# Kernel optimization log

Hardware: AMD Instinct MI355X
Metric: run time of the kernel (lower is better)

## Reference

```python
import jax, jax.numpy as jnp
import numpy as np

B, S, D = 2, 2048, 1024
H, DH = 16, 64
FF = 4 * D
EPS = 1e-5
SCALE = 1.0 / np.sqrt(DH)


def setup_inputs() -> dict:
    key = jax.random.key(0)
    ks = jax.random.split(key, 8)
    std = 0.02
    return {
        "x": jax.random.normal(ks[0], (B, S, D), jnp.float32),
        "ln1_g": jnp.ones((D,), jnp.float32),
        "ln1_b": jnp.zeros((D,), jnp.float32),
        "w_qkv": jax.random.normal(ks[1], (D, 3 * H * DH), jnp.float32) * std,
        "b_qkv": jnp.zeros((3 * H * DH,), jnp.float32),
        "w_ao": jax.random.normal(ks[2], (H * DH, D), jnp.float32) * std,
        "b_ao": jnp.zeros((D,), jnp.float32),
        "ln2_g": jnp.ones((D,), jnp.float32),
        "ln2_b": jnp.zeros((D,), jnp.float32),
        "w_fc": jax.random.normal(ks[3], (D, FF), jnp.float32) * std,
        "b_fc": jnp.zeros((FF,), jnp.float32),
        "w_proj": jax.random.normal(ks[4], (FF, D), jnp.float32) * std,
        "b_proj": jnp.zeros((D,), jnp.float32),
    }


def _layernorm(x, g, b):
    mu = jnp.mean(x, axis=-1, keepdims=True)
    var = jnp.mean(jnp.square(x - mu), axis=-1, keepdims=True)
    return (x - mu) * jax.lax.rsqrt(var + EPS) * g + b


def reference(x, ln1_g, ln1_b, w_qkv, b_qkv, w_ao, b_ao,
              ln2_g, ln2_b, w_fc, b_fc, w_proj, b_proj):
    # pre-LN attention
    h = _layernorm(x, ln1_g, ln1_b)
    qkv = h @ w_qkv + b_qkv                      # [B,S,3*H*DH]
    q, k, v = jnp.split(qkv, 3, axis=-1)
    def heads(t):                                 # [B,S,H*DH] -> [B,H,S,DH]
        return t.reshape(B, S, H, DH).transpose(0, 2, 1, 3)
    q, k, v = heads(q), heads(k), heads(v)
    scores = jnp.einsum("bhsd,bhtd->bhst", q, k) * SCALE  # full [B,H,S,S]
    probs = jax.nn.softmax(scores, axis=-1)
    attn = jnp.einsum("bhst,bhtd->bhsd", probs, v)        # [B,H,S,DH]
    attn = attn.transpose(0, 2, 1, 3).reshape(B, S, H * DH)
    attn = attn @ w_ao + b_ao
    x = x + attn
    # pre-LN MLP (exact erf GELU, matches nn.GELU())
    h = _layernorm(x, ln2_g, ln2_b)
    h = jax.nn.gelu(h @ w_fc + b_fc, approximate=False)
    h = h @ w_proj + b_proj
    return x + h
```

## Files before the change

kernel.cpp:

```cpp
#include <hip/hip_runtime.h>
#include <hip/hip_bf16.h>

using short8 = __attribute__((ext_vector_type(8))) short;
using f32x4  = __attribute__((ext_vector_type(4))) float;

#define DEV __device__ __forceinline__

DEV unsigned short f2b(float f) {
  union { float f; unsigned u; } cv; cv.f = f;
  unsigned r = (cv.u + 0x7fffu + ((cv.u >> 16) & 1u)) >> 16;
  return (unsigned short)r;
}

typedef const __attribute__((address_space(1))) unsigned int* gp1;
typedef __attribute__((address_space(3))) unsigned int* lp3;
DEV void gl16(const void* g, void* l) {
  __builtin_amdgcn_global_load_lds((gp1)g, (lp3)l, 16, 0, 0);
}

__global__ void k_tcvt4(const float* __restrict__ s0, unsigned short* __restrict__ d0,
                        const float* __restrict__ s1, unsigned short* __restrict__ d1,
                        const float* __restrict__ s2, unsigned short* __restrict__ d2,
                        const float* __restrict__ s3, unsigned short* __restrict__ d3) {
  __shared__ float tile[32][33];
  int id = blockIdx.x;
  const float* src; unsigned short* dst; int K, N, nx;
  if (id < 3072)      { src = s0; dst = d0; K = 1024; N = 3072; nx = 96; }
  else if (id < 4096) { id -= 3072; src = s1; dst = d1; K = 1024; N = 1024; nx = 32; }
  else if (id < 8192) { id -= 4096; src = s2; dst = d2; K = 1024; N = 4096; nx = 128; }
  else                { id -= 8192; src = s3; dst = d3; K = 4096; N = 1024; nx = 32; }
  int n0 = (id % nx) * 32, k0 = (id / nx) * 32;
  int tx = threadIdx.x, ty = threadIdx.y;
#pragma unroll
  for (int j = 0; j < 4; ++j)
    tile[ty + j * 8][tx] = src[(size_t)(k0 + ty + j * 8) * N + (n0 + tx)];
  __syncthreads();
#pragma unroll
  for (int j = 0; j < 4; ++j)
    dst[(size_t)(n0 + ty + j * 8) * K + (k0 + tx)] = f2b(tile[tx][ty + j * 8]);
}

__global__ void k_tv(const unsigned short* __restrict__ src, unsigned short* __restrict__ dst) {
  __shared__ unsigned short tile[32][33];
  int d0 = blockIdx.x * 32, s0 = blockIdx.y * 32;
  size_t base = (size_t)blockIdx.z * 2048 * 64;
  int tx = threadIdx.x, ty = threadIdx.y;
#pragma unroll
  for (int j = 0; j < 4; ++j)
    tile[ty + j * 8][tx] = src[base + (size_t)(s0 + ty + j * 8) * 64 + (d0 + tx)];
  __syncthreads();
#pragma unroll
  for (int j = 0; j < 4; ++j)
    dst[base + (size_t)(d0 + ty + j * 8) * 2048 + (s0 + tx)] = tile[tx][ty + j * 8];
}

__global__ __launch_bounds__(256) void k_ln(const float* __restrict__ x,
                                            const float* __restrict__ g,
                                            const float* __restrict__ b,
                                            unsigned short* __restrict__ y) {
  int row = blockIdx.x, tid = threadIdx.x;
  float4 v = reinterpret_cast<const float4*>(x + (size_t)row * 1024)[tid];
  float s  = v.x + v.y + v.z + v.w;
  float s2 = v.x * v.x + v.y * v.y + v.z * v.z + v.w * v.w;
#pragma unroll
  for (int m = 1; m < 64; m <<= 1) { s += __shfl_xor(s, m); s2 += __shfl_xor(s2, m); }
  __shared__ float ps[8];
  int w = tid >> 6;
  if ((tid & 63) == 0) { ps[w] = s; ps[4 + w] = s2; }
  __syncthreads();
  s  = ps[0] + ps[1] + ps[2] + ps[3];
  s2 = ps[4] + ps[5] + ps[6] + ps[7];
  float mu   = s * (1.0f / 1024.0f);
  float var  = fmaxf(s2 * (1.0f / 1024.0f) - mu * mu, 0.f);
  float rstd = rsqrtf(var + 1e-5f);
  float4 gv = reinterpret_cast<const float4*>(g)[tid];
  float4 bv = reinterpret_cast<const float4*>(b)[tid];
  ushort4 o;
  o.x = f2b((v.x - mu) * rstd * gv.x + bv.x);
  o.y = f2b((v.y - mu) * rstd * gv.y + bv.y);
  o.z = f2b((v.z - mu) * rstd * gv.z + bv.z);
  o.w = f2b((v.w - mu) * rstd * gv.w + bv.w);
  reinterpret_cast<ushort4*>(y + (size_t)row * 1024)[tid] = o;
}

enum { EPI_QKV = 0, EPI_RESID = 1, EPI_GELU = 2 };

template <int EPI>
__global__ __launch_bounds__(512, 2) void k_gemm256(
    const unsigned short* __restrict__ A, const unsigned short* __restrict__ BT,
    const float* __restrict__ bias, int M, int N, int K,
    unsigned short* __restrict__ outb,
    unsigned short* __restrict__ qb, unsigned short* __restrict__ kb,
    unsigned short* __restrict__ vb) {
  __shared__ __align__(16) unsigned short Abuf[2][256][64];
  __shared__ __align__(16) unsigned short Bbuf[2][256][64];
  int nx = gridDim.x, nwg = nx * gridDim.y;
  int w0 = blockIdx.y * nx + blockIdx.x;
  int id = (w0 & 7) * (nwg >> 3) + (w0 >> 3);
  int bx = id % nx, by = id / nx;
  int m0 = by * 256, n0 = bx * 256;
  int tid = threadIdx.x;
  int lane = tid & 63, wid = tid >> 6;
  int wm = wid >> 2, wn = wid & 3;
  int l15 = lane & 15, g = lane >> 4;
  int swl = l15 & 7;
  int lrow = lane >> 3;
  int lchunk = (lane & 7) ^ lrow;
  const unsigned short* Asrc = A  + (size_t)(m0 + wid * 32 + lrow) * K + lchunk * 8;
  const unsigned short* Bsrc = BT + (size_t)(n0 + wid * 32 + lrow) * K + lchunk * 8;
  auto stage = [&](int buf, int k0) {
#pragma unroll
    for (int i = 0; i < 4; ++i)
      gl16(Asrc + k0 + (size_t)i * 8 * K, &Abuf[buf][wid * 32 + i * 8][0]);
#pragma unroll
    for (int i = 0; i < 4; ++i)
      gl16(Bsrc + k0 + (size_t)i * 8 * K, &Bbuf[buf][wid * 32 + i * 8][0]);
  };
  f32x4 acc[8][4] = {};
  int nt = K >> 6;
  stage(0, 0);
  stage(1, 64);
  asm volatile("s_waitcnt vmcnt(8)" ::: "memory");
  __builtin_amdgcn_sched_barrier(0);
  __builtin_amdgcn_s_barrier();
  int cur = 0;
  for (int t = 0; t < nt; ++t) {
    const unsigned short (*As)[64] = Abuf[cur];
    const unsigned short (*Bs)[64] = Bbuf[cur];
    short8 a0[8], b0[4], a1[8], b1[4];
#pragma unroll
    for (int mi = 0; mi < 8; ++mi)
      a0[mi] = *reinterpret_cast<const short8*>(&As[wm * 128 + mi * 16 + l15][(g ^ swl) * 8]);
#pragma unroll
    for (int ni = 0; ni < 4; ++ni)
      b0[ni] = *reinterpret_cast<const short8*>(&Bs[wn * 64 + ni * 16 + l15][(g ^ swl) * 8]);
    __builtin_amdgcn_s_setprio(1);
#pragma unroll
    for (int mi = 0; mi < 8; ++mi)
#pragma unroll
      for (int ni = 0; ni < 4; ++ni)
        acc[mi][ni] = __builtin_amdgcn_mfma_f32_16x16x32_bf16(a0[mi], b0[ni], acc[mi][ni], 0, 0, 0);
    __builtin_amdgcn_s_setprio(0);
#pragma unroll
    for (int mi = 0; mi < 8; ++mi)
      a1[mi] = *reinterpret_cast<const short8*>(&As[wm * 128 + mi * 16 + l15][((4 + g) ^ swl) * 8]);
#pragma unroll
    for (int ni = 0; ni < 4; ++ni)
      b1[ni] = *reinterpret_cast<const short8*>(&Bs[wn * 64 + ni * 16 + l15][((4 + g) ^ swl) * 8]);
    asm volatile("s_waitcnt lgkmcnt(0)" ::: "memory");
    __builtin_amdgcn_sched_barrier(0);
    __builtin_amdgcn_s_barrier();
    __builtin_amdgcn_sched_barrier(0);
    if (t + 2 < nt) stage(cur, (t + 2) << 6);
    __builtin_amdgcn_s_setprio(1);
#pragma unroll
    for (int mi = 0; mi < 8; ++mi)
#pragma unroll
      for (int ni = 0; ni < 4; ++ni)
        acc[mi][ni] = __builtin_amdgcn_mfma_f32_16x16x32_bf16(a1[mi], b1[ni], acc[mi][ni], 0, 0, 0);
    __builtin_amdgcn_s_setprio(0);
    if (t + 2 < nt) {
      asm volatile("s_waitcnt vmcnt(8)" ::: "memory");
    } else if (t + 1 < nt) {
      asm volatile("s_waitcnt vmcnt(0)" ::: "memory");
    }
    __builtin_amdgcn_sched_barrier(0);
    __builtin_amdgcn_s_barrier();
    cur ^= 1;
  }
#pragma unroll
  for (int mi = 0; mi < 8; ++mi) {
#pragma unroll
    for (int ni = 0; ni < 4; ++ni) {
      int row0 = m0 + wm * 128 + mi * 16 + g * 4;
      int col  = n0 + wn * 64 + ni * 16 + l15;
      float bcol = bias[col];
#pragma unroll
      for (int j = 0; j < 4; ++j) {
        int r = row0 + j;
        float vv = acc[mi][ni][j] + bcol;
        if (EPI == EPI_QKV) {
          int which = col >> 10;
          int hc = col & 1023;
          int h = hc >> 6, d = hc & 63;
          int bb = r >> 11, ss = r & 2047;
          size_t idx = (((size_t)(bb * 16 + h)) * 2048 + ss) * 64 + d;
          unsigned short bv_ = f2b(which == 0 ? vv * 0.18033688011112042f : vv);
          if (which == 0)      qb[idx] = bv_;
          else if (which == 1) kb[idx] = bv_;
          else                 vb[idx] = bv_;
        } else {
          float ge = 0.5f * vv * (1.0f + erff(vv * 0.70710678118654752f));
          outb[(size_t)r * N + col] = f2b(ge);
        }
      }
    }
  }
}

__global__ __launch_bounds__(512) void k_gemm512(
    const unsigned short* __restrict__ A, const unsigned short* __restrict__ BT,
    const float* __restrict__ bias, int M, int N, int K,
    float* __restrict__ outf, const float* __restrict__ resid) {
  __shared__ __align__(16) unsigned short Abuf[2][64][64];
  __shared__ __align__(16) unsigned short Bbuf[2][128][64];
  int nx = gridDim.x, nwg = nx * gridDim.y;
  int w0 = blockIdx.y * nx + blockIdx.x;
  int id = (w0 & 7) * (nwg >> 3) + (w0 >> 3);
  int bx = id % nx, by = id / nx;
  int m0 = by * 64, n0 = bx * 128;
  int tid = threadIdx.x;
  int lane = tid & 63, wid = tid >> 6;
  int wm = wid >> 2, wn = wid & 3;
  int l15 = lane & 15, g = lane >> 4;
  int swl = l15 & 7;
  int lrow = lane >> 3;
  int lchunk = (lane & 7) ^ lrow;
  const unsigned short* Asrc = A  + (size_t)(m0 + wid * 8 + lrow) * K + lchunk * 8;
  const unsigned short* Bsrc = BT + (size_t)(n0 + wid * 16 + lrow) * K + lchunk * 8;
  auto stage = [&](int buf, int k0) {
    gl16(Asrc + k0, &Abuf[buf][wid * 8][0]);
#pragma unroll
    for (int i = 0; i < 2; ++i)
      gl16(Bsrc + k0 + (size_t)i * 8 * K, &Bbuf[buf][wid * 16 + i * 8][0]);
  };
  f32x4 acc[2][2] = {};
  int nt = K >> 6;
  stage(0, 0);
  stage(1, 64);
  asm volatile("s_waitcnt vmcnt(3)" ::: "memory");
  __builtin_amdgcn_sched_barrier(0);
  __builtin_amdgcn_s_barrier();
  int cur = 0;
  for (int t = 0; t < nt; ++t) {
    const unsigned short (*As)[64] = Abuf[cur];
    const unsigned short (*Bs)[64] = Bbuf[cur];
    short8 a0[2], b0[2], a1[2], b1[2];
#pragma unroll
    for (int mi = 0; mi < 2; ++mi)
      a0[mi] = *reinterpret_cast<const short8*>(&As[wm * 32 + mi * 16 + l15][(g ^ swl) * 8]);
#pragma unroll
    for (int ni = 0; ni < 2; ++ni)
      b0[ni] = *reinterpret_cast<const short8*>(&Bs[wn * 32 + ni * 16 + l15][(g ^ swl) * 8]);
    __builtin_amdgcn_s_setprio(1);
#pragma unroll
    for (int mi = 0; mi < 2; ++mi)
#pragma unroll
      for (int ni = 0; ni < 2; ++ni)
        acc[mi][ni] = __builtin_amdgcn_mfma_f32_16x16x32_bf16(a0[mi], b0[ni], acc[mi][ni], 0, 0, 0);
    __builtin_amdgcn_s_setprio(0);
#pragma unroll
    for (int mi = 0; mi < 2; ++mi)
      a1[mi] = *reinterpret_cast<const short8*>(&As[wm * 32 + mi * 16 + l15][((4 + g) ^ swl) * 8]);
#pragma unroll
    for (int ni = 0; ni < 2; ++ni)
      b1[ni] = *reinterpret_cast<const short8*>(&Bs[wn * 32 + ni * 16 + l15][((4 + g) ^ swl) * 8]);
    asm volatile("s_waitcnt lgkmcnt(0)" ::: "memory");
    __builtin_amdgcn_sched_barrier(0);
    __builtin_amdgcn_s_barrier();
    __builtin_amdgcn_sched_barrier(0);
    if (t + 2 < nt) stage(cur, (t + 2) << 6);
    __builtin_amdgcn_s_setprio(1);
#pragma unroll
    for (int mi = 0; mi < 2; ++mi)
#pragma unroll
      for (int ni = 0; ni < 2; ++ni)
        acc[mi][ni] = __builtin_amdgcn_mfma_f32_16x16x32_bf16(a1[mi], b1[ni], acc[mi][ni], 0, 0, 0);
    __builtin_amdgcn_s_setprio(0);
    if (t + 2 < nt) {
      asm volatile("s_waitcnt vmcnt(3)" ::: "memory");
    } else if (t + 1 < nt) {
      asm volatile("s_waitcnt vmcnt(0)" ::: "memory");
    }
    __builtin_amdgcn_sched_barrier(0);
    __builtin_amdgcn_s_barrier();
    cur ^= 1;
  }
#pragma unroll
  for (int mi = 0; mi < 2; ++mi) {
#pragma unroll
    for (int ni = 0; ni < 2; ++ni) {
      int row0 = m0 + wm * 32 + mi * 16 + g * 4;
      int col  = n0 + wn * 32 + ni * 16 + l15;
      float bcol = bias[col];
#pragma unroll
      for (int j = 0; j < 4; ++j) {
        size_t idx = (size_t)(row0 + j) * N + col;
        outf[idx] = acc[mi][ni][j] + bcol + resid[idx];
      }
    }
  }
}

__global__ __launch_bounds__(256) void k_attn(
    const unsigned short* __restrict__ qb, const unsigned short* __restrict__ kb,
    const unsigned short* __restrict__ vt, unsigned short* __restrict__ attn_out) {
  __shared__ __align__(16) unsigned short Ks[64][64];
  __shared__ __align__(16) unsigned short Vs[64][64];
  __shared__ __align__(16) unsigned short Plds[4][16][72];
  int bh = blockIdx.y;
  int b = bh >> 4, h = bh & 15;
  int tid = threadIdx.x;
  int lane = tid & 63, wid = tid >> 6;
  int l15 = lane & 15, g = lane >> 4;
  int q0 = blockIdx.x * 64 + wid * 16;
  const unsigned short* Qb = qb + (size_t)bh * 2048 * 64;
  const unsigned short* Kb = kb + (size_t)bh * 2048 * 64;
  const unsigned short* Vt = vt + (size_t)bh * 64 * 2048;
  short8 qf0 = *reinterpret_cast<const short8*>(&Qb[(size_t)(q0 + l15) * 64 + g * 8]);
  short8 qf1 = *reinterpret_cast<const short8*>(&Qb[(size_t)(q0 + l15) * 64 + 32 + g * 8]);
  short8 vones;
#pragma unroll
  for (int i = 0; i < 8; ++i) vones[i] = (short)0x3F80;
  float mj = 0.0f;
  f32x4 o[4] = {};
  f32x4 lacc = {};
  int sr  = wid * 16 + (lane >> 3);
  int scn = (lane & 7) ^ (sr & 7);
  int swl = l15 & 7;
  for (int t0 = 0; t0 < 2048; t0 += 64) {
    __syncthreads();
    gl16(Kb + (size_t)(t0 + sr) * 64 + scn * 8,       &Ks[wid * 16][0]);
    gl16(Kb + (size_t)(t0 + sr + 8) * 64 + scn * 8,   &Ks[wid * 16 + 8][0]);
    gl16(Vt + (size_t)sr * 2048 + t0 + scn * 8,       &Vs[wid * 16][0]);
    gl16(Vt + (size_t)(sr + 8) * 2048 + t0 + scn * 8, &Vs[wid * 16 + 8][0]);
    __syncthreads();
    f32x4 scv[4];
#pragma unroll
    for (int kk = 0; kk < 4; ++kk) {
      short8 kf0 = *reinterpret_cast<const short8*>(&Ks[kk * 16 + l15][(g ^ swl) * 8]);
      short8 kf1 = *reinterpret_cast<const short8*>(&Ks[kk * 16 + l15][((4 + g) ^ swl) * 8]);
      f32x4 z = {};
      z = __builtin_amdgcn_mfma_f32_16x16x32_bf16(kf0, qf0, z, 0, 0, 0);
      scv[kk] = __builtin_amdgcn_mfma_f32_16x16x32_bf16(kf1, qf1, z, 0, 0, 0);
    }
    float p[16];
#pragma unroll
    for (int kk = 0; kk < 4; ++kk)
#pragma unroll
      for (int j = 0; j < 4; ++j)
        p[kk * 4 + j] = __builtin_amdgcn_exp2f(scv[kk][j] - mj);
#pragma unroll
    for (int kk = 0; kk < 4; ++kk) {
      unsigned r0, r1;
      asm("v_cvt_pk_bf16_f32 %0, %1, %2" : "=v"(r0) : "v"(p[kk * 4 + 0]), "v"(p[kk * 4 + 1]));
      asm("v_cvt_pk_bf16_f32 %0, %1, %2" : "=v"(r1) : "v"(p[kk * 4 + 2]), "v"(p[kk * 4 + 3]));
      unsigned long long w = (unsigned long long)r0 | ((unsigned long long)r1 << 32);
      *reinterpret_cast<unsigned long long*>(&Plds[wid][l15][kk * 16 + g * 4]) = w;
    }
    float t0m = fmaxf(fmaxf(scv[0][0], scv[0][1]), fmaxf(scv[0][2], scv[0][3]));
    float t1m = fmaxf(fmaxf(scv[1][0], scv[1][1]), fmaxf(scv[1][2], scv[1][3]));
    float t2m = fmaxf(fmaxf(scv[2][0], scv[2][1]), fmaxf(scv[2][2], scv[2][3]));
    float t3m = fmaxf(fmaxf(scv[3][0], scv[3][1]), fmaxf(scv[3][2], scv[3][3]));
    float mx = fmaxf(fmaxf(t0m, t1m), fmaxf(t2m, t3m));
    mx = fmaxf(mx, __shfl_xor(mx, 16));
    mx = fmaxf(mx, __shfl_xor(mx, 32));
    if (!__all(mx <= mj + 8.0f)) {
      float mnew = fmaxf(mj, mx);
      float ef = __builtin_amdgcn_exp2f(mj - mnew);
      int sb = 20 * g;
      float e0 = __shfl(ef, sb + 0), e1 = __shfl(ef, sb + 1);
      float e2 = __shfl(ef, sb + 2), e3 = __shfl(ef, sb + 3);
#pragma unroll
      for (int ct = 0; ct < 4; ++ct) {
        o[ct][0] *= e0; o[ct][1] *= e1; o[ct][2] *= e2; o[ct][3] *= e3;
      }
      lacc[0] *= e0; lacc[1] *= e1; lacc[2] *= e2; lacc[3] *= e3;
#pragma unroll
      for (int kk = 0; kk < 4; ++kk) {
#pragma unroll
        for (int j = 0; j < 4; ++j)
          p[kk * 4 + j] = __builtin_amdgcn_exp2f(scv[kk][j] - mnew);
        unsigned r0, r1;
        asm("v_cvt_pk_bf16_f32 %0, %1, %2" : "=v"(r0) : "v"(p[kk * 4 + 0]), "v"(p[kk * 4 + 1]));
        asm("v_cvt_pk_bf16_f32 %0, %1, %2" : "=v"(r1) : "v"(p[kk * 4 + 2]), "v"(p[kk * 4 + 3]));
        unsigned long long w = (unsigned long long)r0 | ((unsigned long long)r1 << 32);
        *reinterpret_cast<unsigned long long*>(&Plds[wid][l15][kk * 16 + g * 4]) = w;
      }
      mj = mnew;
    }
    short8 pf0 = *reinterpret_cast<const short8*>(&Plds[wid][l15][g * 8]);
    short8 pf1 = *reinterpret_cast<const short8*>(&Plds[wid][l15][32 + g * 8]);
    lacc = __builtin_amdgcn_mfma_f32_16x16x32_bf16(pf0, vones, lacc, 0, 0, 0);
    lacc = __builtin_amdgcn_mfma_f32_16x16x32_bf16(pf1, vones, lacc, 0, 0, 0);
#pragma unroll
    for (int ct = 0; ct < 4; ++ct) {
      short8 vf0 = *reinterpret_cast<const short8*>(&Vs[ct * 16 + l15][(g ^ swl) * 8]);
      short8 vf1 = *reinterpret_cast<const short8*>(&Vs[ct * 16 + l15][((4 + g) ^ swl) * 8]);
      o[ct] = __builtin_amdgcn_mfma_f32_16x16x32_bf16(pf0, vf0, o[ct], 0, 0, 0);
      o[ct] = __builtin_amdgcn_mfma_f32_16x16x32_bf16(pf1, vf1, o[ct], 0, 0, 0);
    }
  }
#pragma unroll
  for (int j = 0; j < 4; ++j) {
    float iv = 1.0f / lacc[j];
    size_t t = (size_t)b * 2048 + (q0 + g * 4 + j);
#pragma unroll
    for (int ct = 0; ct < 4; ++ct)
      attn_out[t * 1024 + h * 64 + ct * 16 + l15] = f2b(o[ct][j] * iv);
  }
}

extern "C" void kernel_launch(void* const* d_in, const int* in_sizes, int n_in,
                              void* d_out, int out_size, void* d_ws, size_t ws_size,
                              hipStream_t stream) {
  (void)in_sizes; (void)n_in; (void)out_size; (void)ws_size;
  const float* x      = (const float*)d_in[0];
  const float* ln1_g  = (const float*)d_in[1];
  const float* ln1_b  = (const float*)d_in[2];
  const float* w_qkv  = (const float*)d_in[3];
  const float* b_qkv  = (const float*)d_in[4];
  const float* w_ao   = (const float*)d_in[5];
  const float* b_ao   = (const float*)d_in[6];
  const float* ln2_g  = (const float*)d_in[7];
  const float* ln2_b  = (const float*)d_in[8];
  const float* w_fc   = (const float*)d_in[9];
  const float* b_fc   = (const float*)d_in[10];
  const float* w_proj = (const float*)d_in[11];
  const float* b_proj = (const float*)d_in[12];
  float* out = (float*)d_out;

  char* ws = (char*)d_ws;
  size_t o = 0;
  auto nxt = [&](size_t bytes) { void* p = ws + o; o += (bytes + 255) & ~(size_t)255; return p; };
  unsigned short* wT_qkv  = (unsigned short*)nxt((size_t)3072 * 1024 * 2);
  unsigned short* wT_ao   = (unsigned short*)nxt((size_t)1024 * 1024 * 2);
  unsigned short* wT_fc   = (unsigned short*)nxt((size_t)4096 * 1024 * 2);
  unsigned short* wT_proj = (unsigned short*)nxt((size_t)1024 * 4096 * 2);
  unsigned short* h_ln    = (unsigned short*)nxt((size_t)4096 * 1024 * 2);
  unsigned short* qbuf    = (unsigned short*)nxt((size_t)4096 * 1024 * 2);
  unsigned short* kbuf    = (unsigned short*)nxt((size_t)4096 * 1024 * 2);
  unsigned short* vbuf    = (unsigned short*)nxt((size_t)4096 * 1024 * 2);
  unsigned short* vtb     = (unsigned short*)nxt((size_t)4096 * 1024 * 2);
  float*          out1    = (float*)nxt((size_t)4096 * 1024 * 4);
  unsigned short* fc_buf  = qbuf;
  unsigned short* attn_o  = vbuf;

  dim3 b32(32, 8, 1);
  k_tcvt4<<<12288, b32, 0, stream>>>(w_qkv, wT_qkv, w_ao, wT_ao, w_fc, wT_fc, w_proj, wT_proj);

  k_ln<<<4096, 256, 0, stream>>>(x, ln1_g, ln1_b, h_ln);
  k_gemm256<EPI_QKV><<<dim3(12, 16), 512, 0, stream>>>(h_ln, wT_qkv, b_qkv, 4096, 3072, 1024,
                                                       nullptr, qbuf, kbuf, vbuf);
  k_tv<<<dim3(2, 64, 32), b32, 0, stream>>>(vbuf, vtb);
  k_attn<<<dim3(32, 32), 256, 0, stream>>>(qbuf, kbuf, vtb, attn_o);
  k_gemm512<<<dim3(8, 64), 512, 0, stream>>>(attn_o, wT_ao, b_ao, 4096, 1024, 1024,
                                             out1, x);
  k_ln<<<4096, 256, 0, stream>>>(out1, ln2_g, ln2_b, h_ln);
  k_gemm256<EPI_GELU><<<dim3(16, 16), 512, 0, stream>>>(h_ln, wT_fc, b_fc, 4096, 4096, 1024,
                                                        fc_buf, nullptr, nullptr, nullptr);
  k_gemm512<<<dim3(8, 64), 512, 0, stream>>>(fc_buf, wT_proj, b_proj, 4096, 1024, 4096,
                                             out, out1);
}
```

Before: 239.2 us.

## Write V transposed from QKV GEMM epilogue and widen attention blocks to 8 waves

```diff
diff --git a/kernel.cpp b/kernel.cpp
--- a/kernel.cpp
+++ b/kernel.cpp
@@ -38,20 +38,6 @@
 #pragma unroll
   for (int j = 0; j < 4; ++j)
     dst[(size_t)(n0 + ty + j * 8) * K + (k0 + tx)] = f2b(tile[tx][ty + j * 8]);
-}
-
-__global__ void k_tv(const unsigned short* __restrict__ src, unsigned short* __restrict__ dst) {
-  __shared__ unsigned short tile[32][33];
-  int d0 = blockIdx.x * 32, s0 = blockIdx.y * 32;
-  size_t base = (size_t)blockIdx.z * 2048 * 64;
-  int tx = threadIdx.x, ty = threadIdx.y;
-#pragma unroll
-  for (int j = 0; j < 4; ++j)
-    tile[ty + j * 8][tx] = src[base + (size_t)(s0 + ty + j * 8) * 64 + (d0 + tx)];
-  __syncthreads();
-#pragma unroll
-  for (int j = 0; j < 4; ++j)
-    dst[base + (size_t)(d0 + ty + j * 8) * 2048 + (s0 + tx)] = tile[tx][ty + j * 8];
 }
 
 __global__ __launch_bounds__(256) void k_ln(const float* __restrict__ x,
@@ -175,23 +161,34 @@
       int row0 = m0 + wm * 128 + mi * 16 + g * 4;
       int col  = n0 + wn * 64 + ni * 16 + l15;
       float bcol = bias[col];
-#pragma unroll
-      for (int j = 0; j < 4; ++j) {
-        int r = row0 + j;
-        float vv = acc[mi][ni][j] + bcol;
-        if (EPI == EPI_QKV) {
-          int which = col >> 10;
-          int hc = col & 1023;
-          int h = hc >> 6, d = hc & 63;
-          int bb = r >> 11, ss = r & 2047;
-          size_t idx = (((size_t)(bb * 16 + h)) * 2048 + ss) * 64 + d;
-          unsigned short bv_ = f2b(which == 0 ? vv * 0.18033688011112042f : vv);
-          if (which == 0)      qb[idx] = bv_;
-          else if (which == 1) kb[idx] = bv_;
-          else                 vb[idx] = bv_;
+      if (EPI == EPI_QKV) {
+        int which = col >> 10;
+        int hc = col & 1023;
+        int h = hc >> 6, d = hc & 63;
+        int bb = row0 >> 11, ss0 = row0 & 2047;
+        if (which == 2) {
+          ushort4 pk;
+          pk.x = f2b(acc[mi][ni][0] + bcol);
+          pk.y = f2b(acc[mi][ni][1] + bcol);
+          pk.z = f2b(acc[mi][ni][2] + bcol);
+          pk.w = f2b(acc[mi][ni][3] + bcol);
+          *reinterpret_cast<ushort4*>(&vb[(((size_t)(bb * 16 + h)) * 64 + d) * 2048 + ss0]) = pk;
         } else {
+#pragma unroll
+          for (int j = 0; j < 4; ++j) {
+            float vv = acc[mi][ni][j] + bcol;
+            size_t idx = (((size_t)(bb * 16 + h)) * 2048 + ss0 + j) * 64 + d;
+            unsigned short bv_ = f2b(which == 0 ? vv * 0.18033688011112042f : vv);
+            if (which == 0) qb[idx] = bv_;
+            else            kb[idx] = bv_;
+          }
+        }
+      } else {
+#pragma unroll
+        for (int j = 0; j < 4; ++j) {
+          float vv = acc[mi][ni][j] + bcol;
           float ge = 0.5f * vv * (1.0f + erff(vv * 0.70710678118654752f));
-          outb[(size_t)r * N + col] = f2b(ge);
+          outb[(size_t)(row0 + j) * N + col] = f2b(ge);
         }
       }
     }
@@ -292,18 +289,18 @@
   }
 }
 
-__global__ __launch_bounds__(256) void k_attn(
+__global__ __launch_bounds__(512) void k_attn(
     const unsigned short* __restrict__ qb, const unsigned short* __restrict__ kb,
     const unsigned short* __restrict__ vt, unsigned short* __restrict__ attn_out) {
   __shared__ __align__(16) unsigned short Ks[64][64];
   __shared__ __align__(16) unsigned short Vs[64][64];
-  __shared__ __align__(16) unsigned short Plds[4][16][72];
+  __shared__ __align__(16) unsigned short Plds[8][16][72];
   int bh = blockIdx.y;
   int b = bh >> 4, h = bh & 15;
   int tid = threadIdx.x;
   int lane = tid & 63, wid = tid >> 6;
   int l15 = lane & 15, g = lane >> 4;
-  int q0 = blockIdx.x * 64 + wid * 16;
+  int q0 = blockIdx.x * 128 + wid * 16;
   const unsigned short* Qb = qb + (size_t)bh * 2048 * 64;
   const unsigned short* Kb = kb + (size_t)bh * 2048 * 64;
   const unsigned short* Vt = vt + (size_t)bh * 64 * 2048;
@@ -315,15 +312,13 @@
   float mj = 0.0f;
   f32x4 o[4] = {};
   f32x4 lacc = {};
-  int sr  = wid * 16 + (lane >> 3);
+  int sr  = wid * 8 + (lane >> 3);
   int scn = (lane & 7) ^ (sr & 7);
   int swl = l15 & 7;
   for (int t0 = 0; t0 < 2048; t0 += 64) {
     __syncthreads();
-    gl16(Kb + (size_t)(t0 + sr) * 64 + scn * 8,       &Ks[wid * 16][0]);
-    gl16(Kb + (size_t)(t0 + sr + 8) * 64 + scn * 8,   &Ks[wid * 16 + 8][0]);
-    gl16(Vt + (size_t)sr * 2048 + t0 + scn * 8,       &Vs[wid * 16][0]);
-    gl16(Vt + (size_t)(sr + 8) * 2048 + t0 + scn * 8, &Vs[wid * 16 + 8][0]);
+    gl16(Kb + (size_t)(t0 + sr) * 64 + scn * 8, &Ks[wid * 8][0]);
+    gl16(Vt + (size_t)sr * 2048 + t0 + scn * 8, &Vs[wid * 8][0]);
     __syncthreads();
     f32x4 scv[4];
 #pragma unroll
@@ -430,20 +425,18 @@
   unsigned short* h_ln    = (unsigned short*)nxt((size_t)4096 * 1024 * 2);
   unsigned short* qbuf    = (unsigned short*)nxt((size_t)4096 * 1024 * 2);
   unsigned short* kbuf    = (unsigned short*)nxt((size_t)4096 * 1024 * 2);
-  unsigned short* vbuf    = (unsigned short*)nxt((size_t)4096 * 1024 * 2);
   unsigned short* vtb     = (unsigned short*)nxt((size_t)4096 * 1024 * 2);
+  unsigned short* attn_o  = (unsigned short*)nxt((size_t)4096 * 1024 * 2);
   float*          out1    = (float*)nxt((size_t)4096 * 1024 * 4);
   unsigned short* fc_buf  = qbuf;
-  unsigned short* attn_o  = vbuf;
 
   dim3 b32(32, 8, 1);
   k_tcvt4<<<12288, b32, 0, stream>>>(w_qkv, wT_qkv, w_ao, wT_ao, w_fc, wT_fc, w_proj, wT_proj);
 
   k_ln<<<4096, 256, 0, stream>>>(x, ln1_g, ln1_b, h_ln);
   k_gemm256<EPI_QKV><<<dim3(12, 16), 512, 0, stream>>>(h_ln, wT_qkv, b_qkv, 4096, 3072, 1024,
-                                                       nullptr, qbuf, kbuf, vbuf);
-  k_tv<<<dim3(2, 64, 32), b32, 0, stream>>>(vbuf, vtb);
-  k_attn<<<dim3(32, 32), 256, 0, stream>>>(qbuf, kbuf, vtb, attn_o);
+                                                       nullptr, qbuf, kbuf, vtb);
+  k_attn<<<dim3(16, 32), 512, 0, stream>>>(qbuf, kbuf, vtb, attn_o);
   k_gemm512<<<dim3(8, 64), 512, 0, stream>>>(attn_o, wT_ao, b_ao, 4096, 1024, 1024,
                                              out1, x);
   k_ln<<<4096, 256, 0, stream>>>(out1, ln2_g, ln2_b, h_ln);
```

Result: faster. 228.8 us (-4.4%).
